# Kernel tuning notes

Measured on AMD Instinct MI355X. Metric: run time of the kernel, lower is better.

Reference implementation:

```python
import jax, jax.numpy as jnp
import numpy as np

B, S, D, H = 4, 2048, 768, 12
DH = D // H          # 64 head dim
DF = 4 * D           # 3072 FFN hidden
EPS = 1e-5


def setup_inputs() -> dict:
    key = jax.random.key(0)
    ks = jax.random.split(key, 16)
    s = 0.02
    inp = {
        "Q": jax.random.normal(ks[0], (B, S, D), jnp.float32),
        "K": jax.random.normal(ks[1], (B, S, D), jnp.float32),
        "V": jax.random.normal(ks[2], (B, S, D), jnp.float32),
        "Wq": s * jax.random.normal(ks[3], (D, D), jnp.float32),
        "bq": jnp.zeros((D,), jnp.float32),
        "Wk": s * jax.random.normal(ks[4], (D, D), jnp.float32),
        "bk": jnp.zeros((D,), jnp.float32),
        "Wv": s * jax.random.normal(ks[5], (D, D), jnp.float32),
        "bv": jnp.zeros((D,), jnp.float32),
        "Wo": s * jax.random.normal(ks[6], (D, D), jnp.float32),
        "bo": jnp.zeros((D,), jnp.float32),
        "ln_g": jnp.ones((D,), jnp.float32),
        "ln_b": jnp.zeros((D,), jnp.float32),
        "W1": s * jax.random.normal(ks[7], (D, DF), jnp.float32),
        "b1": jnp.zeros((DF,), jnp.float32),
        "W2": s * jax.random.normal(ks[8], (DF, D), jnp.float32),
        "b2": jnp.zeros((D,), jnp.float32),
    }
    return inp


def _split_heads(x):  # [B,S,D] -> [B,H,S,DH]
    return x.reshape(B, S, H, DH).transpose(0, 2, 1, 3)


def _layernorm(x, g, b):
    mu = jnp.mean(x, axis=-1, keepdims=True)
    var = jnp.mean(jnp.square(x - mu), axis=-1, keepdims=True)
    return (x - mu) * jax.lax.rsqrt(var + EPS) * g + b


def reference(Q, K, V, Wq, bq, Wk, bk, Wv, bv, Wo, bo, ln_g, ln_b, W1, b1, W2, b2):
    q = _split_heads(Q @ Wq + bq)            # [B,H,S,DH]
    k = _split_heads(K @ Wk + bk)
    v = _split_heads(V @ Wv + bv)
    scale = 1.0 / jnp.sqrt(jnp.asarray(DH, q.dtype))
    scores = jnp.einsum("bhqd,bhkd->bhqk", q, k) * scale   # [B,H,S,S]
    attn = jax.nn.softmax(scores, axis=-1)
    ctx = jnp.einsum("bhqk,bhkd->bhqd", attn, v)            # [B,H,S,DH]
    ctx = ctx.transpose(0, 2, 1, 3).reshape(B, S, D)
    attn_out = ctx @ Wo + bo
    h = _layernorm(Q + attn_out, ln_g, ln_b)                # residual + LN
    ff = jax.nn.gelu(h @ W1 + b1, approximate=False) @ W2 + b2
    return ff
```

## Files before the change

kernel.cpp:

```cpp
#include <hip/hip_runtime.h>
#include <hip/hip_bf16.h>
#include <math.h>

#define Bsz 4
#define Ssz 2048
#define Dsz 768
#define Hn  12
#define DHn 64
#define DFn 3072
#define NTOK (Bsz*Ssz)
#define EPSL 1e-5f

typedef __attribute__((ext_vector_type(8))) short bf16x8;
typedef __attribute__((ext_vector_type(4))) float f32x4;

__device__ __forceinline__ unsigned short f2bf(float f) {
    unsigned int u = __float_as_uint(f);
    u += 0x7fffu + ((u >> 16) & 1u);
    return (unsigned short)(u >> 16);
}
__device__ __forceinline__ float bf2f(unsigned short h) {
    return __uint_as_float(((unsigned int)h) << 16);
}

__device__ __forceinline__ void swizzle_mn(int bid, int mtot, int nb, int& m, int& n)
{
    const int xcd = bid & 7;
    const int idx = bid >> 3;
    m = xcd * (mtot >> 3) + idx / nb;
    n = idx % nb;
}

__global__ __launch_bounds__(256)
void wsplit_k(const float* __restrict__ W, unsigned short* __restrict__ Wh,
              unsigned short* __restrict__ Wl, int K, int N)
{
    __shared__ float tile[32][33];
    const int n0 = blockIdx.x * 32, k0 = blockIdx.y * 32;
    const int x = threadIdx.x, y = threadIdx.y;
    #pragma unroll
    for (int i = 0; i < 4; i++)
        tile[y + 8 * i][x] = W[(size_t)(k0 + y + 8 * i) * N + n0 + x];
    __syncthreads();
    #pragma unroll
    for (int i = 0; i < 4; i++) {
        float v = tile[x][y + 8 * i];
        unsigned short hb = f2bf(v);
        size_t o = (size_t)(n0 + y + 8 * i) * K + k0 + x;
        Wh[o] = hb;
        Wl[o] = f2bf(v - bf2f(hb));
    }
}

__global__ __launch_bounds__(256)
void presplit_k(const float* __restrict__ Qf, const float* __restrict__ Kf,
                const float* __restrict__ Vf,
                unsigned short* __restrict__ Qh, unsigned short* __restrict__ Ql,
                unsigned short* __restrict__ Kh, unsigned short* __restrict__ Kl,
                unsigned short* __restrict__ Vh)
{
    const int blocksPerSeg = (NTOK * Dsz) / 2048;
    const int seg = blockIdx.x / blocksPerSeg;
    const int idx = ((blockIdx.x % blocksPerSeg) * 256 + threadIdx.x) * 8;
    const float* src = (seg == 0) ? Qf : (seg == 1) ? Kf : Vf;

    float4 a = *(const float4*)(src + idx);
    float4 b = *(const float4*)(src + idx + 4);
    float fv[8] = {a.x, a.y, a.z, a.w, b.x, b.y, b.z, b.w};

    bf16x8 h8, l8;
    #pragma unroll
    for (int e = 0; e < 8; e++) {
        unsigned short hb = f2bf(fv[e]);
        h8[e] = (short)hb;
        l8[e] = (short)f2bf(fv[e] - bf2f(hb));
    }
    unsigned short* Hp = (seg == 0) ? Qh : (seg == 1) ? Kh : Vh;
    *(bf16x8*)(Hp + idx) = h8;
    if (seg < 2) {
        unsigned short* Lp = (seg == 0) ? Ql : Kl;
        *(bf16x8*)(Lp + idx) = l8;
    }
}

__global__ __launch_bounds__(256)
void qkv_mfma(const unsigned short* __restrict__ Qsh, const unsigned short* __restrict__ Qsl,
              const unsigned short* __restrict__ Ksh, const unsigned short* __restrict__ Ksl,
              const unsigned short* __restrict__ Vsh,
              const unsigned short* __restrict__ Wqh, const unsigned short* __restrict__ Wql,
              const unsigned short* __restrict__ Wkh, const unsigned short* __restrict__ Wkl,
              const unsigned short* __restrict__ Wvh, const unsigned short* __restrict__ Wvl,
              const float* __restrict__ bq, const float* __restrict__ bk,
              const float* __restrict__ bv,
              unsigned short* __restrict__ qh, unsigned short* __restrict__ ql,
              unsigned short* __restrict__ kh, unsigned short* __restrict__ kl,
              unsigned short* __restrict__ vout)
{
    __shared__ short smem[16384];
    short* As_h = smem;
    short* As_l = smem + 4096;
    short* Bs_h = smem + 8192;
    short* Bs_l = smem + 12288;

    const int t    = threadIdx.x;
    const int lane = t & 63;
    const int w    = t >> 6;
    const int wm   = w >> 1;
    const int wn   = w & 1;

    int m_tile, nblk;
    swizzle_mn(blockIdx.x, 192, 6, m_tile, nblk);
    const int which = m_tile / 64;
    const int m0    = (m_tile % 64) * 128;
    const int n0    = nblk * 128;

    const unsigned short* Ah = (which == 0) ? Qsh : (which == 1) ? Ksh : Vsh;
    const unsigned short* Al = (which == 0) ? Qsl : Ksl;
    const unsigned short* Bh = (which == 0) ? Wqh : (which == 1) ? Wkh : Wvh;
    const unsigned short* Bl = (which == 0) ? Wql : (which == 1) ? Wkl : Wvl;
    const float* bias = (which == 0) ? bq : (which == 1) ? bk : bv;

    f32x4 acc[4][4];
    #pragma unroll
    for (int i = 0; i < 4; i++)
        #pragma unroll
        for (int j = 0; j < 4; j++)
            acc[i][j] = (f32x4){0.f, 0.f, 0.f, 0.f};

    const int fr = lane & 15;
    const int q8 = (lane >> 4) * 8;

    for (int k0 = 0; k0 < Dsz; k0 += 32) {
        __syncthreads();
        #pragma unroll
        for (int it = 0; it < 2; it++) {
            const int p   = t + 256 * it;
            const int row = p >> 2;
            const int c8  = (p & 3) * 8;
            const unsigned short* ga_h = Ah + (size_t)(m0 + row) * Dsz + k0 + c8;
            const unsigned short* gb_h = Bh + (size_t)(n0 + row) * Dsz + k0 + c8;
            __builtin_amdgcn_global_load_lds((const __attribute__((address_space(1))) void*)ga_h,
                (__attribute__((address_space(3))) void*)(As_h + p * 8), 16, 0, 0);
            __builtin_amdgcn_global_load_lds((const __attribute__((address_space(1))) void*)gb_h,
                (__attribute__((address_space(3))) void*)(Bs_h + p * 8), 16, 0, 0);
            if (which < 2) {
                const unsigned short* ga_l = Al + (size_t)(m0 + row) * Dsz + k0 + c8;
                const unsigned short* gb_l = Bl + (size_t)(n0 + row) * Dsz + k0 + c8;
                __builtin_amdgcn_global_load_lds((const __attribute__((address_space(1))) void*)ga_l,
                    (__attribute__((address_space(3))) void*)(As_l + p * 8), 16, 0, 0);
                __builtin_amdgcn_global_load_lds((const __attribute__((address_space(1))) void*)gb_l,
                    (__attribute__((address_space(3))) void*)(Bs_l + p * 8), 16, 0, 0);
            }
        }
        __syncthreads();

        bf16x8 a_h[4], a_l[4], b_h[4], b_l[4];
        #pragma unroll
        for (int i = 0; i < 4; i++) {
            const int ra = (wm * 64 + i * 16 + fr) * 32 + q8;
            const int rb = (wn * 64 + i * 16 + fr) * 32 + q8;
            a_h[i] = *(const bf16x8*)&As_h[ra];
            b_h[i] = *(const bf16x8*)&Bs_h[rb];
            if (which < 2) {
                a_l[i] = *(const bf16x8*)&As_l[ra];
                b_l[i] = *(const bf16x8*)&Bs_l[rb];
            }
        }
        if (which < 2) {
            #pragma unroll
            for (int i = 0; i < 4; i++)
                #pragma unroll
                for (int j = 0; j < 4; j++) {
                    acc[i][j] = __builtin_amdgcn_mfma_f32_16x16x32_bf16(a_l[i], b_h[j], acc[i][j], 0, 0, 0);
                    acc[i][j] = __builtin_amdgcn_mfma_f32_16x16x32_bf16(a_h[i], b_l[j], acc[i][j], 0, 0, 0);
                    acc[i][j] = __builtin_amdgcn_mfma_f32_16x16x32_bf16(a_h[i], b_h[j], acc[i][j], 0, 0, 0);
                }
        } else {
            #pragma unroll
            for (int i = 0; i < 4; i++)
                #pragma unroll
                for (int j = 0; j < 4; j++)
                    acc[i][j] = __builtin_amdgcn_mfma_f32_16x16x32_bf16(a_h[i], b_h[j], acc[i][j], 0, 0, 0);
        }
    }

    const int quad = lane >> 4;
    #pragma unroll
    for (int i = 0; i < 4; i++)
        #pragma unroll
        for (int j = 0; j < 4; j++) {
            const int n  = n0 + wn * 64 + j * 16 + fr;
            const float bn = bias[n];
            const int hh = n >> 6, dh = n & 63;
            #pragma unroll
            for (int r = 0; r < 4; r++) {
                const int m = m0 + wm * 64 + i * 16 + quad * 4 + r;
                const int bb = m >> 11, s = m & 2047;
                const size_t o = (((size_t)bb * Hn + hh) * Ssz + s) * DHn + dh;
                float v = acc[i][j][r] + bn;
                if (which == 0) {
                    v *= 0.125f;
                    unsigned short hb = f2bf(v);
                    qh[o] = hb; ql[o] = f2bf(v - bf2f(hb));
                } else if (which == 1) {
                    unsigned short hb = f2bf(v);
                    kh[o] = hb; kl[o] = f2bf(v - bf2f(hb));
                } else {
                    vout[o] = f2bf(v);
                }
            }
        }
}

__global__ __launch_bounds__(256)
void vtrans_k(const unsigned short* __restrict__ src, unsigned short* __restrict__ dst)
{
    __shared__ unsigned short tl[32][33];
    const int s0 = blockIdx.x * 32;
    const int d0 = blockIdx.y * 32;
    const int hd = blockIdx.z;
    const int x = threadIdx.x, y = threadIdx.y;
    const size_t base = (size_t)hd * Ssz * DHn;
    #pragma unroll
    for (int i = 0; i < 4; i++)
        tl[y + 8 * i][x] = src[base + (size_t)(s0 + y + 8 * i) * DHn + d0 + x];
    __syncthreads();
    #pragma unroll
    for (int i = 0; i < 4; i++)
        dst[base + (size_t)(d0 + y + 8 * i) * Ssz + s0 + x] = tl[x][y + 8 * i];
}

template<int MODE, bool ASPLIT, bool BSPLIT>
__global__ __launch_bounds__(256)
void gemm_mfma(const unsigned short* __restrict__ Ah, const unsigned short* __restrict__ Al,
               const unsigned short* __restrict__ Bh, const unsigned short* __restrict__ Bl,
               const float* __restrict__ bias, const float* __restrict__ res,
               float* __restrict__ Cf, unsigned short* __restrict__ Cb,
               int M, int N, int K)
{
    __shared__ short smem[16384];
    short* As_h = smem;
    short* As_l = smem + 4096;
    short* Bs_h = smem + 8192;
    short* Bs_l = smem + 12288;

    const int t    = threadIdx.x;
    const int lane = t & 63;
    const int w    = t >> 6;
    const int wm   = w >> 1;
    const int wn   = w & 1;

    int mt, nt_;
    swizzle_mn(blockIdx.x, M >> 7, N >> 7, mt, nt_);
    const int m0 = mt * 128;
    const int n0 = nt_ * 128;

    f32x4 acc[4][4];
    #pragma unroll
    for (int i = 0; i < 4; i++)
        #pragma unroll
        for (int j = 0; j < 4; j++)
            acc[i][j] = (f32x4){0.f, 0.f, 0.f, 0.f};

    const int fr = lane & 15;
    const int q8 = (lane >> 4) * 8;

    for (int k0 = 0; k0 < K; k0 += 32) {
        __syncthreads();
        #pragma unroll
        for (int it = 0; it < 2; it++) {
            const int p   = t + 256 * it;
            const int row = p >> 2;
            const int c8  = (p & 3) * 8;
            const unsigned short* ga_h = Ah + (size_t)(m0 + row) * K + k0 + c8;
            const unsigned short* gb_h = Bh + (size_t)(n0 + row) * K + k0 + c8;
            __builtin_amdgcn_global_load_lds((const __attribute__((address_space(1))) void*)ga_h,
                (__attribute__((address_space(3))) void*)(As_h + p * 8), 16, 0, 0);
            if (ASPLIT) {
                const unsigned short* ga_l = Al + (size_t)(m0 + row) * K + k0 + c8;
                __builtin_amdgcn_global_load_lds((const __attribute__((address_space(1))) void*)ga_l,
                    (__attribute__((address_space(3))) void*)(As_l + p * 8), 16, 0, 0);
            }
            __builtin_amdgcn_global_load_lds((const __attribute__((address_space(1))) void*)gb_h,
                (__attribute__((address_space(3))) void*)(Bs_h + p * 8), 16, 0, 0);
            if (BSPLIT) {
                const unsigned short* gb_l = Bl + (size_t)(n0 + row) * K + k0 + c8;
                __builtin_amdgcn_global_load_lds((const __attribute__((address_space(1))) void*)gb_l,
                    (__attribute__((address_space(3))) void*)(Bs_l + p * 8), 16, 0, 0);
            }
        }
        __syncthreads();

        bf16x8 a_h[4], a_l[4], b_h[4], b_l[4];
        #pragma unroll
        for (int i = 0; i < 4; i++) {
            const int ra = (wm * 64 + i * 16 + fr) * 32 + q8;
            const int rb = (wn * 64 + i * 16 + fr) * 32 + q8;
            a_h[i] = *(const bf16x8*)&As_h[ra];
            if (ASPLIT) a_l[i] = *(const bf16x8*)&As_l[ra];
            b_h[i] = *(const bf16x8*)&Bs_h[rb];
            if (BSPLIT) b_l[i] = *(const bf16x8*)&Bs_l[rb];
        }
        #pragma unroll
        for (int i = 0; i < 4; i++)
            #pragma unroll
            for (int j = 0; j < 4; j++) {
                if (ASPLIT)
                    acc[i][j] = __builtin_amdgcn_mfma_f32_16x16x32_bf16(a_l[i], b_h[j], acc[i][j], 0, 0, 0);
                if (BSPLIT)
                    acc[i][j] = __builtin_amdgcn_mfma_f32_16x16x32_bf16(a_h[i], b_l[j], acc[i][j], 0, 0, 0);
                acc[i][j] = __builtin_amdgcn_mfma_f32_16x16x32_bf16(a_h[i], b_h[j], acc[i][j], 0, 0, 0);
            }
    }

    const int quad = lane >> 4;
    #pragma unroll
    for (int i = 0; i < 4; i++)
        #pragma unroll
        for (int j = 0; j < 4; j++) {
            const int n  = n0 + wn * 64 + j * 16 + fr;
            const float bn = bias[n];
            #pragma unroll
            for (int r = 0; r < 4; r++) {
                const int m = m0 + wm * 64 + i * 16 + quad * 4 + r;
                float v = acc[i][j][r] + bn;
                if (MODE == 1) {
                    v += res[(size_t)m * N + n];
                    Cf[(size_t)m * N + n] = v;
                } else if (MODE == 2) {
                    v = 0.5f * v * (1.0f + erff(v * 0.70710678118654752f));
                    Cb[(size_t)m * N + n] = f2bf(v);
                } else {
                    Cf[(size_t)m * N + n] = v;
                }
            }
        }
}

__device__ __forceinline__ void stage16(const unsigned short* src, short* dst,
                                        int p0, int lane, int row0, int rstride, int col0)
{
    const int p   = p0 + lane;
    const int n   = p >> 3;
    const int cst = (p & 7) ^ (n & 7);
    const unsigned short* g = src + (size_t)(row0 + n) * rstride + col0 + cst * 8;
    __builtin_amdgcn_global_load_lds((const __attribute__((address_space(1))) void*)g,
        (__attribute__((address_space(3))) void*)(dst + p0 * 8), 16, 0, 0);
}

__device__ __forceinline__ bf16x8 frag(const short* arr, int row, int c)
{
    const int pos = row * 8 + (c ^ (row & 7));
    return *(const bf16x8*)&arr[pos * 8];
}

__global__ __launch_bounds__(256)
void attn_mfma(const unsigned short* __restrict__ qh, const unsigned short* __restrict__ ql,
               const unsigned short* __restrict__ kh, const unsigned short* __restrict__ kl,
               const unsigned short* __restrict__ vt, unsigned short* __restrict__ ch)
{
    const int hid = blockIdx.x;
    const int b   = hid / Hn;
    const int h   = hid - b * Hn;
    const int q0  = blockIdx.y * 64;
    const int t    = threadIdx.x;
    const int lane = t & 63;
    const int w    = t >> 6;
    const int fr   = lane & 15;
    const int quad = lane >> 4;

    __shared__ short sKV[12288];
    __shared__ short sQP[8192];
    short* Kh_s = sKV;
    short* Kl_s = sKV + 4096;
    short* Vh_s = sKV + 8192;
    short* Qh_s = sQP;
    short* Ql_s = sQP + 4096;
    float* Pw   = (float*)sQP + w * 1024;

    const size_t hoff = (size_t)hid * Ssz * DHn;

    stage16(qh + hoff, Qh_s, w * 128,      lane, q0, DHn, 0);
    stage16(qh + hoff, Qh_s, w * 128 + 64, lane, q0, DHn, 0);
    stage16(ql + hoff, Ql_s, w * 128,      lane, q0, DHn, 0);
    stage16(ql + hoff, Ql_s, w * 128 + 64, lane, q0, DHn, 0);

    f32x4 O[4];
    #pragma unroll
    for (int d = 0; d < 4; d++) O[d] = (f32x4){0.f, 0.f, 0.f, 0.f};
    float lp[4] = {0.f, 0.f, 0.f, 0.f};

    bf16x8 qfh[2], qfl[2];

    for (int kt = 0; kt < Ssz / 64; kt++) {
        __syncthreads();
        const int kr = kt * 64;
        #pragma unroll
        for (int bt = 0; bt < 2; bt++) {
            const int p0 = w * 128 + bt * 64;
            stage16(kh + hoff, Kh_s, p0, lane, kr, DHn, 0);
            stage16(kl + hoff, Kl_s, p0, lane, kr, DHn, 0);
            stage16(vt + hoff, Vh_s, p0, lane, 0, Ssz, kr);
        }
        __syncthreads();

        if (kt == 0) {
            #pragma unroll
            for (int kc = 0; kc < 2; kc++) {
                qfh[kc] = frag(Qh_s, w * 16 + fr, kc * 4 + quad);
                qfl[kc] = frag(Ql_s, w * 16 + fr, kc * 4 + quad);
            }
            __syncthreads();
        }

        f32x4 sc[4];
        #pragma unroll
        for (int nt = 0; nt < 4; nt++) sc[nt] = (f32x4){0.f, 0.f, 0.f, 0.f};
        __builtin_amdgcn_s_setprio(1);
        #pragma unroll
        for (int nt = 0; nt < 4; nt++)
            #pragma unroll
            for (int kc = 0; kc < 2; kc++) {
                bf16x8 bh = frag(Kh_s, nt * 16 + fr, kc * 4 + quad);
                bf16x8 bl = frag(Kl_s, nt * 16 + fr, kc * 4 + quad);
                sc[nt] = __builtin_amdgcn_mfma_f32_16x16x32_bf16(qfl[kc], bh, sc[nt], 0, 0, 0);
                sc[nt] = __builtin_amdgcn_mfma_f32_16x16x32_bf16(qfh[kc], bl, sc[nt], 0, 0, 0);
                sc[nt] = __builtin_amdgcn_mfma_f32_16x16x32_bf16(qfh[kc], bh, sc[nt], 0, 0, 0);
            }
        __builtin_amdgcn_s_setprio(0);

        #pragma unroll
        for (int r = 0; r < 4; r++) {
            const int m = quad * 4 + r;
            #pragma unroll
            for (int nt = 0; nt < 4; nt++) {
                float p = __expf(sc[nt][r]);
                const int j  = nt * 16 + fr;
                const int c4 = j >> 2;
                Pw[(m * 16 + (c4 ^ m)) * 4 + (j & 3)] = p;
                lp[r] += p;
            }
        }

        #pragma unroll
        for (int kc = 0; kc < 2; kc++) {
            const int c4a = kc * 8 + quad * 2;
            float4 pa = *(float4*)&Pw[(fr * 16 + (c4a ^ fr)) * 4];
            float4 pb = *(float4*)&Pw[(fr * 16 + ((c4a + 1) ^ fr)) * 4];
            union { bf16x8 v; __hip_bfloat162 b2[4]; } P;
            P.b2[0] = __float22bfloat162_rn(make_float2(pa.x, pa.y));
            P.b2[1] = __float22bfloat162_rn(make_float2(pa.z, pa.w));
            P.b2[2] = __float22bfloat162_rn(make_float2(pb.x, pb.y));
            P.b2[3] = __float22bfloat162_rn(make_float2(pb.z, pb.w));
            __builtin_amdgcn_s_setprio(1);
            #pragma unroll
            for (int dt = 0; dt < 4; dt++) {
                bf16x8 vh = frag(Vh_s, dt * 16 + fr, kc * 4 + quad);
                O[dt] = __builtin_amdgcn_mfma_f32_16x16x32_bf16(P.v, vh, O[dt], 0, 0, 0);
            }
            __builtin_amdgcn_s_setprio(0);
        }
    }

    #pragma unroll
    for (int r = 0; r < 4; r++) {
        float ls = lp[r];
        #pragma unroll
        for (int msk = 1; msk < 16; msk <<= 1) ls += __shfl_xor(ls, msk);
        const float linv = 1.0f / ls;
        const int s = q0 + w * 16 + quad * 4 + r;
        unsigned short* och = ch + ((size_t)b * Ssz + s) * Dsz + h * DHn;
        #pragma unroll
        for (int dt = 0; dt < 4; dt++)
            och[dt * 16 + fr] = f2bf(O[dt][r] * linv);
    }
}

__global__ __launch_bounds__(256)
void ln_k(const float* __restrict__ x, const float* __restrict__ g,
          const float* __restrict__ bb, unsigned short* __restrict__ yh)
{
    const int row = blockIdx.x;
    const float* xr = x + (size_t)row * Dsz;
    unsigned short* yhr = yh + (size_t)row * Dsz;
    const int t = threadIdx.x;

    float v0 = xr[t], v1 = xr[t + 256], v2 = xr[t + 512];
    float s = v0 + v1 + v2;
    #pragma unroll
    for (int o = 1; o < 64; o <<= 1) s += __shfl_xor(s, o, 64);

    __shared__ float red1[4];
    __shared__ float red2[4];
    const int wid = t >> 6, lane = t & 63;
    if (lane == 0) red1[wid] = s;
    __syncthreads();
    const float mean = (red1[0] + red1[1] + red1[2] + red1[3]) * (1.0f / Dsz);

    float d0 = v0 - mean, d1 = v1 - mean, d2 = v2 - mean;
    float vs = d0 * d0 + d1 * d1 + d2 * d2;
    #pragma unroll
    for (int o = 1; o < 64; o <<= 1) vs += __shfl_xor(vs, o, 64);
    if (lane == 0) red2[wid] = vs;
    __syncthreads();
    const float var = (red2[0] + red2[1] + red2[2] + red2[3]) * (1.0f / Dsz);
    const float inv = rsqrtf(var + EPSL);

    yhr[t]       = f2bf(d0 * inv * g[t]       + bb[t]);
    yhr[t + 256] = f2bf(d1 * inv * g[t + 256] + bb[t + 256]);
    yhr[t + 512] = f2bf(d2 * inv * g[t + 512] + bb[t + 512]);
}

extern "C" void kernel_launch(void* const* d_in, const int* in_sizes, int n_in,
                              void* d_out, int out_size, void* d_ws, size_t ws_size,
                              hipStream_t stream)
{
    (void)in_sizes; (void)n_in; (void)out_size; (void)ws_size;
    const float* Q    = (const float*)d_in[0];
    const float* Kin  = (const float*)d_in[1];
    const float* Vin  = (const float*)d_in[2];
    const float* Wq   = (const float*)d_in[3];
    const float* bq   = (const float*)d_in[4];
    const float* Wk   = (const float*)d_in[5];
    const float* bk   = (const float*)d_in[6];
    const float* Wv   = (const float*)d_in[7];
    const float* bv   = (const float*)d_in[8];
    const float* Wo   = (const float*)d_in[9];
    const float* bo   = (const float*)d_in[10];
    const float* ln_g = (const float*)d_in[11];
    const float* ln_b = (const float*)d_in[12];
    const float* W1   = (const float*)d_in[13];
    const float* b1   = (const float*)d_in[14];
    const float* W2   = (const float*)d_in[15];
    const float* b2   = (const float*)d_in[16];
    float* out = (float*)d_out;

    const size_t NT = (size_t)NTOK * Dsz;
    unsigned short* usws = (unsigned short*)d_ws;
    unsigned short* qh  = usws + 0 * NT;
    unsigned short* ql  = usws + 1 * NT;
    unsigned short* kh  = usws + 2 * NT;
    unsigned short* kl  = usws + 3 * NT;
    unsigned short* vt  = usws + 4 * NT;
    unsigned short* ch  = usws + 6 * NT;
    unsigned short* wsp = usws + 8 * NT;
    const size_t SW = (size_t)Dsz * Dsz;
    unsigned short* Wqh = wsp + 0 * SW;
    unsigned short* Wql = wsp + 1 * SW;
    unsigned short* Wkh = wsp + 2 * SW;
    unsigned short* Wkl = wsp + 3 * SW;
    unsigned short* Wvh = wsp + 4 * SW;
    unsigned short* Wvl = wsp + 5 * SW;
    unsigned short* Woh = wsp + 6 * SW;
    unsigned short* Wol = wsp + 7 * SW;
    unsigned short* W1h = wsp + 8 * SW;
    unsigned short* W1l = wsp + 12 * SW;
    unsigned short* W2h = wsp + 16 * SW;
    unsigned short* W2l = wsp + 20 * SW;
    float*          hpre = (float*)usws;
    unsigned short* hh   = kh;
    unsigned short* hbuf = usws + 4 * NT;

    unsigned short* Qsh = usws + 4 * NT;
    unsigned short* Qsl = usws + 5 * NT;
    unsigned short* Ksh = usws + 7 * NT;
    unsigned short* Ksl = (unsigned short*)d_out;
    unsigned short* Vsh = (unsigned short*)d_out + NT;

    dim3 wb(32, 8);
    wsplit_k<<<dim3(Dsz / 32, Dsz / 32), wb, 0, stream>>>(Wq, Wqh, Wql, Dsz, Dsz);
    wsplit_k<<<dim3(Dsz / 32, Dsz / 32), wb, 0, stream>>>(Wk, Wkh, Wkl, Dsz, Dsz);
    wsplit_k<<<dim3(Dsz / 32, Dsz / 32), wb, 0, stream>>>(Wv, Wvh, Wvl, Dsz, Dsz);
    wsplit_k<<<dim3(Dsz / 32, Dsz / 32), wb, 0, stream>>>(Wo, Woh, Wol, Dsz, Dsz);
    wsplit_k<<<dim3(DFn / 32, Dsz / 32), wb, 0, stream>>>(W1, W1h, W1l, Dsz, DFn);
    wsplit_k<<<dim3(Dsz / 32, DFn / 32), wb, 0, stream>>>(W2, W2h, W2l, DFn, Dsz);

    presplit_k<<<3 * (NTOK * Dsz / 2048), 256, 0, stream>>>(
        Q, Kin, Vin, Qsh, Qsl, Ksh, Ksl, Vsh);

    qkv_mfma<<<1152, 256, 0, stream>>>(
        Qsh, Qsl, Ksh, Ksl, Vsh,
        Wqh, Wql, Wkh, Wkl, Wvh, Wvl, bq, bk, bv,
        qh, ql, kh, kl, ch);

    vtrans_k<<<dim3(Ssz / 32, DHn / 32, Bsz * Hn), wb, 0, stream>>>(ch, vt);

    attn_mfma<<<dim3(Bsz * Hn, Ssz / 64), 256, 0, stream>>>(qh, ql, kh, kl, vt, ch);

    gemm_mfma<1, false, true><<<384, 256, 0, stream>>>(
        ch, nullptr, Woh, Wol, bo, Q, hpre, nullptr, NTOK, Dsz, Dsz);

    ln_k<<<NTOK, 256, 0, stream>>>(hpre, ln_g, ln_b, hh);

    gemm_mfma<2, false, true><<<1536, 256, 0, stream>>>(
        hh, nullptr, W1h, W1l, b1, nullptr, nullptr, hbuf, NTOK, DFn, Dsz);
    gemm_mfma<3, false, false><<<384, 256, 0, stream>>>(
        hbuf, nullptr, W2h, nullptr, b2, nullptr, out, nullptr, NTOK, Dsz, DFn);
}
```

Before: 631.5 us.

## Compute transposed scores so P stays in registers via shuffles, dropping LDS round-trip

The QK^T MFMA swaps operands so each lane holds scores along the key dimension for one query column. The exponentiated probabilities are then packed to bf16 pairs and redistributed across lanes with shuffles to form the PV A-operand, instead of writing floats to LDS and reading them back. The Q/P shared buffer is removed, Q is staged through the K buffer, and the row-sum reduction is simplified. The aim is to cut LDS traffic and shared memory use, raising occupancy, at the cost of extra cross-lane shuffles and selects.

```diff
diff --git a/kernel.cpp b/kernel.cpp
--- a/kernel.cpp
+++ b/kernel.cpp
@@ -370,27 +370,33 @@
     const int quad = lane >> 4;
 
     __shared__ short sKV[12288];
-    __shared__ short sQP[8192];
     short* Kh_s = sKV;
     short* Kl_s = sKV + 4096;
     short* Vh_s = sKV + 8192;
-    short* Qh_s = sQP;
-    short* Ql_s = sQP + 4096;
-    float* Pw   = (float*)sQP + w * 1024;
 
     const size_t hoff = (size_t)hid * Ssz * DHn;
 
-    stage16(qh + hoff, Qh_s, w * 128,      lane, q0, DHn, 0);
-    stage16(qh + hoff, Qh_s, w * 128 + 64, lane, q0, DHn, 0);
-    stage16(ql + hoff, Ql_s, w * 128,      lane, q0, DHn, 0);
-    stage16(ql + hoff, Ql_s, w * 128 + 64, lane, q0, DHn, 0);
+    stage16(qh + hoff, Kh_s, w * 128,      lane, q0, DHn, 0);
+    stage16(qh + hoff, Kh_s, w * 128 + 64, lane, q0, DHn, 0);
+    stage16(ql + hoff, Kl_s, w * 128,      lane, q0, DHn, 0);
+    stage16(ql + hoff, Kl_s, w * 128 + 64, lane, q0, DHn, 0);
+    __syncthreads();
+
+    bf16x8 qfh[2], qfl[2];
+    #pragma unroll
+    for (int kc = 0; kc < 2; kc++) {
+        qfh[kc] = frag(Kh_s, w * 16 + fr, kc * 4 + quad);
+        qfl[kc] = frag(Kl_s, w * 16 + fr, kc * 4 + quad);
+    }
 
     f32x4 O[4];
     #pragma unroll
     for (int d = 0; d < 4; d++) O[d] = (f32x4){0.f, 0.f, 0.f, 0.f};
-    float lp[4] = {0.f, 0.f, 0.f, 0.f};
-
-    bf16x8 qfh[2], qfl[2];
+    float lp = 0.f;
+
+    const int s0l = fr + ((quad & 1) << 5);
+    const int s1l = s0l + 16;
+    const bool hi2 = (quad >> 1) != 0;
 
     for (int kt = 0; kt < Ssz / 64; kt++) {
         __syncthreads();
@@ -404,15 +410,6 @@
         }
         __syncthreads();
 
-        if (kt == 0) {
-            #pragma unroll
-            for (int kc = 0; kc < 2; kc++) {
-                qfh[kc] = frag(Qh_s, w * 16 + fr, kc * 4 + quad);
-                qfl[kc] = frag(Ql_s, w * 16 + fr, kc * 4 + quad);
-            }
-            __syncthreads();
-        }
-
         f32x4 sc[4];
         #pragma unroll
         for (int nt = 0; nt < 4; nt++) sc[nt] = (f32x4){0.f, 0.f, 0.f, 0.f};
@@ -421,53 +418,60 @@
         for (int nt = 0; nt < 4; nt++)
             #pragma unroll
             for (int kc = 0; kc < 2; kc++) {
-                bf16x8 bh = frag(Kh_s, nt * 16 + fr, kc * 4 + quad);
-                bf16x8 bl = frag(Kl_s, nt * 16 + fr, kc * 4 + quad);
-                sc[nt] = __builtin_amdgcn_mfma_f32_16x16x32_bf16(qfl[kc], bh, sc[nt], 0, 0, 0);
-                sc[nt] = __builtin_amdgcn_mfma_f32_16x16x32_bf16(qfh[kc], bl, sc[nt], 0, 0, 0);
-                sc[nt] = __builtin_amdgcn_mfma_f32_16x16x32_bf16(qfh[kc], bh, sc[nt], 0, 0, 0);
+                bf16x8 ah = frag(Kh_s, nt * 16 + fr, kc * 4 + quad);
+                bf16x8 al = frag(Kl_s, nt * 16 + fr, kc * 4 + quad);
+                sc[nt] = __builtin_amdgcn_mfma_f32_16x16x32_bf16(ah, qfl[kc], sc[nt], 0, 0, 0);
+                sc[nt] = __builtin_amdgcn_mfma_f32_16x16x32_bf16(al, qfh[kc], sc[nt], 0, 0, 0);
+                sc[nt] = __builtin_amdgcn_mfma_f32_16x16x32_bf16(ah, qfh[kc], sc[nt], 0, 0, 0);
             }
         __builtin_amdgcn_s_setprio(0);
 
-        #pragma unroll
-        for (int r = 0; r < 4; r++) {
-            const int m = quad * 4 + r;
-            #pragma unroll
-            for (int nt = 0; nt < 4; nt++) {
-                float p = __expf(sc[nt][r]);
-                const int j  = nt * 16 + fr;
-                const int c4 = j >> 2;
-                Pw[(m * 16 + (c4 ^ m)) * 4 + (j & 3)] = p;
-                lp[r] += p;
-            }
+        unsigned int pw0[4], pw1[4];
+        #pragma unroll
+        for (int nt = 0; nt < 4; nt++) {
+            float p0 = __expf(sc[nt][0]);
+            float p1 = __expf(sc[nt][1]);
+            float p2 = __expf(sc[nt][2]);
+            float p3 = __expf(sc[nt][3]);
+            lp += (p0 + p1) + (p2 + p3);
+            __hip_bfloat162 wa = __float22bfloat162_rn(make_float2(p0, p1));
+            __hip_bfloat162 wb = __float22bfloat162_rn(make_float2(p2, p3));
+            pw0[nt] = *reinterpret_cast<unsigned int*>(&wa);
+            pw1[nt] = *reinterpret_cast<unsigned int*>(&wb);
         }
 
         #pragma unroll
         for (int kc = 0; kc < 2; kc++) {
-            const int c4a = kc * 8 + quad * 2;
-            float4 pa = *(float4*)&Pw[(fr * 16 + (c4a ^ fr)) * 4];
-            float4 pb = *(float4*)&Pw[(fr * 16 + ((c4a + 1) ^ fr)) * 4];
-            union { bf16x8 v; __hip_bfloat162 b2[4]; } P;
-            P.b2[0] = __float22bfloat162_rn(make_float2(pa.x, pa.y));
-            P.b2[1] = __float22bfloat162_rn(make_float2(pa.z, pa.w));
-            P.b2[2] = __float22bfloat162_rn(make_float2(pb.x, pb.y));
-            P.b2[3] = __float22bfloat162_rn(make_float2(pb.z, pb.w));
+            union { bf16x8 v; unsigned int u[4]; } PA;
+            unsigned int a0 = (unsigned int)__shfl((int)pw0[kc * 2 + 0], s0l);
+            unsigned int b0 = (unsigned int)__shfl((int)pw0[kc * 2 + 1], s0l);
+            unsigned int a1 = (unsigned int)__shfl((int)pw1[kc * 2 + 0], s0l);
+            unsigned int b1 = (unsigned int)__shfl((int)pw1[kc * 2 + 1], s0l);
+            unsigned int a2 = (unsigned int)__shfl((int)pw0[kc * 2 + 0], s1l);
+            unsigned int b2 = (unsigned int)__shfl((int)pw0[kc * 2 + 1], s1l);
+            unsigned int a3 = (unsigned int)__shfl((int)pw1[kc * 2 + 0], s1l);
+            unsigned int b3 = (unsigned int)__shfl((int)pw1[kc * 2 + 1], s1l);
+            PA.u[0] = hi2 ? b0 : a0;
+            PA.u[1] = hi2 ? b1 : a1;
+            PA.u[2] = hi2 ? b2 : a2;
+            PA.u[3] = hi2 ? b3 : a3;
             __builtin_amdgcn_s_setprio(1);
             #pragma unroll
             for (int dt = 0; dt < 4; dt++) {
                 bf16x8 vh = frag(Vh_s, dt * 16 + fr, kc * 4 + quad);
-                O[dt] = __builtin_amdgcn_mfma_f32_16x16x32_bf16(P.v, vh, O[dt], 0, 0, 0);
+                O[dt] = __builtin_amdgcn_mfma_f32_16x16x32_bf16(PA.v, vh, O[dt], 0, 0, 0);
             }
             __builtin_amdgcn_s_setprio(0);
         }
     }
 
+    lp += __shfl_xor(lp, 16);
+    lp += __shfl_xor(lp, 32);
+    const float linv_all = 1.0f / lp;
+
     #pragma unroll
     for (int r = 0; r < 4; r++) {
-        float ls = lp[r];
-        #pragma unroll
-        for (int msk = 1; msk < 16; msk <<= 1) ls += __shfl_xor(ls, msk);
-        const float linv = 1.0f / ls;
+        const float linv = __shfl(linv_all, quad * 4 + r);
         const int s = q0 + w * 16 + quad * 4 + r;
         unsigned short* och = ch + ((size_t)b * Ssz + s) * Dsz + h * DHn;
         #pragma unroll
```

After: 663.7 us. +5.1%, slower.

## Process two query tiles per attention block to reuse staged K/V

Applied to the files above, without the earlier changes.

Each attention workgroup now handles 128 query rows (two 64-row tiles) instead of 64, holding Q fragments and output accumulators for both tiles in registers. Each K/V tile staged into LDS is used twice, halving global K/V traffic and LDS staging per unit of work. The cost is more registers per thread (possibly lower occupancy) and half as many workgroups (768 instead of 1536), which may underfill the GPU.

```diff
diff --git a/kernel.cpp b/kernel.cpp
--- a/kernel.cpp
+++ b/kernel.cpp
@@ -362,7 +362,7 @@
     const int hid = blockIdx.x;
     const int b   = hid / Hn;
     const int h   = hid - b * Hn;
-    const int q0  = blockIdx.y * 64;
+    const int q0  = blockIdx.y * 128;
     const int t    = threadIdx.x;
     const int lane = t & 63;
     const int w    = t >> 6;
@@ -384,13 +384,31 @@
     stage16(qh + hoff, Qh_s, w * 128 + 64, lane, q0, DHn, 0);
     stage16(ql + hoff, Ql_s, w * 128,      lane, q0, DHn, 0);
     stage16(ql + hoff, Ql_s, w * 128 + 64, lane, q0, DHn, 0);
-
-    f32x4 O[4];
-    #pragma unroll
-    for (int d = 0; d < 4; d++) O[d] = (f32x4){0.f, 0.f, 0.f, 0.f};
-    float lp[4] = {0.f, 0.f, 0.f, 0.f};
-
-    bf16x8 qfh[2], qfl[2];
+    __syncthreads();
+    bf16x8 qfh[2][2], qfl[2][2];
+    #pragma unroll
+    for (int kc = 0; kc < 2; kc++) {
+        qfh[0][kc] = frag(Qh_s, w * 16 + fr, kc * 4 + quad);
+        qfl[0][kc] = frag(Ql_s, w * 16 + fr, kc * 4 + quad);
+    }
+    __syncthreads();
+    stage16(qh + hoff, Qh_s, w * 128,      lane, q0 + 64, DHn, 0);
+    stage16(qh + hoff, Qh_s, w * 128 + 64, lane, q0 + 64, DHn, 0);
+    stage16(ql + hoff, Ql_s, w * 128,      lane, q0 + 64, DHn, 0);
+    stage16(ql + hoff, Ql_s, w * 128 + 64, lane, q0 + 64, DHn, 0);
+    __syncthreads();
+    #pragma unroll
+    for (int kc = 0; kc < 2; kc++) {
+        qfh[1][kc] = frag(Qh_s, w * 16 + fr, kc * 4 + quad);
+        qfl[1][kc] = frag(Ql_s, w * 16 + fr, kc * 4 + quad);
+    }
+
+    f32x4 O[2][4];
+    #pragma unroll
+    for (int qt = 0; qt < 2; qt++)
+        #pragma unroll
+        for (int d = 0; d < 4; d++) O[qt][d] = (f32x4){0.f, 0.f, 0.f, 0.f};
+    float lp[2][4] = {{0.f, 0.f, 0.f, 0.f}, {0.f, 0.f, 0.f, 0.f}};
 
     for (int kt = 0; kt < Ssz / 64; kt++) {
         __syncthreads();
@@ -404,76 +422,72 @@
         }
         __syncthreads();
 
-        if (kt == 0) {
+        #pragma unroll
+        for (int qt = 0; qt < 2; qt++) {
+            f32x4 sc[4];
+            #pragma unroll
+            for (int nt = 0; nt < 4; nt++) sc[nt] = (f32x4){0.f, 0.f, 0.f, 0.f};
+            __builtin_amdgcn_s_setprio(1);
+            #pragma unroll
+            for (int nt = 0; nt < 4; nt++)
+                #pragma unroll
+                for (int kc = 0; kc < 2; kc++) {
+                    bf16x8 bh = frag(Kh_s, nt * 16 + fr, kc * 4 + quad);
+                    bf16x8 bl = frag(Kl_s, nt * 16 + fr, kc * 4 + quad);
+                    sc[nt] = __builtin_amdgcn_mfma_f32_16x16x32_bf16(qfl[qt][kc], bh, sc[nt], 0, 0, 0);
+                    sc[nt] = __builtin_amdgcn_mfma_f32_16x16x32_bf16(qfh[qt][kc], bl, sc[nt], 0, 0, 0);
+                    sc[nt] = __builtin_amdgcn_mfma_f32_16x16x32_bf16(qfh[qt][kc], bh, sc[nt], 0, 0, 0);
+                }
+            __builtin_amdgcn_s_setprio(0);
+
+            #pragma unroll
+            for (int r = 0; r < 4; r++) {
+                const int m = quad * 4 + r;
+                #pragma unroll
+                for (int nt = 0; nt < 4; nt++) {
+                    float p = __expf(sc[nt][r]);
+                    const int j  = nt * 16 + fr;
+                    const int c4 = j >> 2;
+                    Pw[(m * 16 + (c4 ^ m)) * 4 + (j & 3)] = p;
+                    lp[qt][r] += p;
+                }
+            }
+
             #pragma unroll
             for (int kc = 0; kc < 2; kc++) {
-                qfh[kc] = frag(Qh_s, w * 16 + fr, kc * 4 + quad);
-                qfl[kc] = frag(Ql_s, w * 16 + fr, kc * 4 + quad);
-            }
-            __syncthreads();
-        }
-
-        f32x4 sc[4];
-        #pragma unroll
-        for (int nt = 0; nt < 4; nt++) sc[nt] = (f32x4){0.f, 0.f, 0.f, 0.f};
-        __builtin_amdgcn_s_setprio(1);
-        #pragma unroll
-        for (int nt = 0; nt < 4; nt++)
-            #pragma unroll
-            for (int kc = 0; kc < 2; kc++) {
-                bf16x8 bh = frag(Kh_s, nt * 16 + fr, kc * 4 + quad);
-                bf16x8 bl = frag(Kl_s, nt * 16 + fr, kc * 4 + quad);
-                sc[nt] = __builtin_amdgcn_mfma_f32_16x16x32_bf16(qfl[kc], bh, sc[nt], 0, 0, 0);
-                sc[nt] = __builtin_amdgcn_mfma_f32_16x16x32_bf16(qfh[kc], bl, sc[nt], 0, 0, 0);
-                sc[nt] = __builtin_amdgcn_mfma_f32_16x16x32_bf16(qfh[kc], bh, sc[nt], 0, 0, 0);
-            }
-        __builtin_amdgcn_s_setprio(0);
-
+                const int c4a = kc * 8 + quad * 2;
+                float4 pa = *(float4*)&Pw[(fr * 16 + (c4a ^ fr)) * 4];
+                float4 pb = *(float4*)&Pw[(fr * 16 + ((c4a + 1) ^ fr)) * 4];
+                union { bf16x8 v; __hip_bfloat162 b2[4]; } P;
+                P.b2[0] = __float22bfloat162_rn(make_float2(pa.x, pa.y));
+                P.b2[1] = __float22bfloat162_rn(make_float2(pa.z, pa.w));
+                P.b2[2] = __float22bfloat162_rn(make_float2(pb.x, pb.y));
+                P.b2[3] = __float22bfloat162_rn(make_float2(pb.z, pb.w));
+                __builtin_amdgcn_s_setprio(1);
+                #pragma unroll
+                for (int dt = 0; dt < 4; dt++) {
+                    bf16x8 vh = frag(Vh_s, dt * 16 + fr, kc * 4 + quad);
+                    O[qt][dt] = __builtin_amdgcn_mfma_f32_16x16x32_bf16(P.v, vh, O[qt][dt], 0, 0, 0);
+                }
+                __builtin_amdgcn_s_setprio(0);
+            }
+        }
+    }
+
+    #pragma unroll
+    for (int qt = 0; qt < 2; qt++)
         #pragma unroll
         for (int r = 0; r < 4; r++) {
-            const int m = quad * 4 + r;
-            #pragma unroll
-            for (int nt = 0; nt < 4; nt++) {
-                float p = __expf(sc[nt][r]);
-                const int j  = nt * 16 + fr;
-                const int c4 = j >> 2;
-                Pw[(m * 16 + (c4 ^ m)) * 4 + (j & 3)] = p;
-                lp[r] += p;
-            }
-        }
-
-        #pragma unroll
-        for (int kc = 0; kc < 2; kc++) {
-            const int c4a = kc * 8 + quad * 2;
-            float4 pa = *(float4*)&Pw[(fr * 16 + (c4a ^ fr)) * 4];
-            float4 pb = *(float4*)&Pw[(fr * 16 + ((c4a + 1) ^ fr)) * 4];
-            union { bf16x8 v; __hip_bfloat162 b2[4]; } P;
-            P.b2[0] = __float22bfloat162_rn(make_float2(pa.x, pa.y));
-            P.b2[1] = __float22bfloat162_rn(make_float2(pa.z, pa.w));
-            P.b2[2] = __float22bfloat162_rn(make_float2(pb.x, pb.y));
-            P.b2[3] = __float22bfloat162_rn(make_float2(pb.z, pb.w));
-            __builtin_amdgcn_s_setprio(1);
-            #pragma unroll
-            for (int dt = 0; dt < 4; dt++) {
-                bf16x8 vh = frag(Vh_s, dt * 16 + fr, kc * 4 + quad);
-                O[dt] = __builtin_amdgcn_mfma_f32_16x16x32_bf16(P.v, vh, O[dt], 0, 0, 0);
-            }
-            __builtin_amdgcn_s_setprio(0);
-        }
-    }
-
-    #pragma unroll
-    for (int r = 0; r < 4; r++) {
-        float ls = lp[r];
-        #pragma unroll
-        for (int msk = 1; msk < 16; msk <<= 1) ls += __shfl_xor(ls, msk);
-        const float linv = 1.0f / ls;
-        const int s = q0 + w * 16 + quad * 4 + r;
-        unsigned short* och = ch + ((size_t)b * Ssz + s) * Dsz + h * DHn;
-        #pragma unroll
-        for (int dt = 0; dt < 4; dt++)
-            och[dt * 16 + fr] = f2bf(O[dt][r] * linv);
-    }
+            float ls = lp[qt][r];
+            #pragma unroll
+            for (int msk = 1; msk < 16; msk <<= 1) ls += __shfl_xor(ls, msk);
+            const float linv = 1.0f / ls;
+            const int s = q0 + qt * 64 + w * 16 + quad * 4 + r;
+            unsigned short* och = ch + ((size_t)b * Ssz + s) * Dsz + h * DHn;
+            #pragma unroll
+            for (int dt = 0; dt < 4; dt++)
+                och[dt * 16 + fr] = f2bf(O[qt][dt][r] * linv);
+        }
 }
 
 __global__ __launch_bounds__(256)
@@ -585,7 +599,7 @@
 
     vtrans_k<<<dim3(Ssz / 32, DHn / 32, Bsz * Hn), wb, 0, stream>>>(ch, vt);
 
-    attn_mfma<<<dim3(Bsz * Hn, Ssz / 64), 256, 0, stream>>>(qh, ql, kh, kl, vt, ch);
+    attn_mfma<<<dim3(Bsz * Hn, Ssz / 128), 256, 0, stream>>>(qh, ql, kh, kl, vt, ch);
 
     gemm_mfma<1, false, true><<<384, 256, 0, stream>>>(
         ch, nullptr, Woh, Wol, bo, Q, hpre, nullptr, NTOK, Dsz, Dsz);
```

Result: slower. 651.1 us (+3.1%).
